# Kernel tuning notes

Measured on AMD Instinct MI355X. Metric: run time of the kernel, lower is better.

The kernel has to match this reference:

```python
import jax, jax.numpy as jnp
import numpy as np

N = 50000
E = 800000
IN_DIM = 512
H1 = IN_DIM // 2   # 256
H2 = IN_DIM // 4   # 128
D = 8
NP_CAYLEY = D * (D - 1) // 2  # 28


def setup_inputs() -> dict:
    key = jax.random.key(0)
    ks = jax.random.split(key, 10)
    x = jax.random.normal(ks[0], (N, IN_DIM), dtype=jnp.float32)
    edge_index = jax.random.randint(ks[1], (2, E), 0, N, dtype=jnp.int64)
    s1 = 1.0 / np.sqrt(IN_DIM)
    s2 = 1.0 / np.sqrt(H1)
    s3 = 1.0 / np.sqrt(H2)
    W1l = jax.random.uniform(ks[2], (H1, IN_DIM), jnp.float32, -s1, s1)
    b1 = jax.random.uniform(ks[3], (H1,), jnp.float32, -s1, s1)
    W1r = jax.random.uniform(ks[4], (H1, IN_DIM), jnp.float32, -s1, s1)
    W2l = jax.random.uniform(ks[5], (H2, H1), jnp.float32, -s2, s2)
    b2 = jax.random.uniform(ks[6], (H2,), jnp.float32, -s2, s2)
    W2r = jax.random.uniform(ks[7], (H2, H1), jnp.float32, -s2, s2)
    Wp = jax.random.uniform(ks[8], (NP_CAYLEY, H2), jnp.float32, -s3, s3)
    bp = jax.random.uniform(ks[9], (NP_CAYLEY,), jnp.float32, -s3, s3)
    return {"x": x, "edge_index": edge_index,
            "W1l": W1l, "b1": b1, "W1r": W1r,
            "W2l": W2l, "b2": b2, "W2r": W2r,
            "Wp": Wp, "bp": bp}


def _sage_conv(x, src, dst, Wl, bl, Wr):
    # PyG SAGEConv (mean aggr): out = lin_l(mean_{j in N(i)} x_j) + lin_r(x_i)
    msg_sum = jax.ops.segment_sum(x[src], dst, num_segments=N)  # [N, F]
    deg = jax.ops.segment_sum(jnp.ones((src.shape[0],), x.dtype), dst,
                              num_segments=N)
    mean = msg_sum / jnp.maximum(deg, 1.0)[:, None]
    return mean @ Wl.T + bl + x @ Wr.T


def _cayley(params):
    # params: [N, d(d-1)/2] -> skew A, then O = (I - A)^{-1} (I + A)
    iu, ju = jnp.triu_indices(D, k=1)  # row-major i<j matches torch loop order
    n = params.shape[0]
    A = jnp.zeros((n, D, D), params.dtype)
    A = A.at[:, iu, ju].set(params)
    A = A.at[:, ju, iu].set(-params)
    I = jnp.eye(D, dtype=params.dtype)
    return jnp.linalg.solve(I[None] - A, I[None] + A)


def reference(x, edge_index, W1l, b1, W1r, W2l, b2, W2r, Wp, bp):
    src, dst = edge_index[0], edge_index[1]
    h = jax.nn.relu(_sage_conv(x, src, dst, W1l, b1, W1r))
    h = jax.nn.relu(_sage_conv(h, src, dst, W2l, b2, W2r))
    params = h @ Wp.T + bp  # [N, 28]
    return _cayley(params)  # [N, 8, 8]
```

## Files before the change

### kernel.cpp

```cpp
#include <hip/hip_runtime.h>
#include <hip/hip_bf16.h>


#define WS_ALIGN(x) (((x) + 255) & ~size_t(255))

typedef __attribute__((ext_vector_type(8))) short short8;
typedef __attribute__((ext_vector_type(4))) float floatx4;

static __device__ __forceinline__ ushort f2b(float f) {
    unsigned u = __builtin_bit_cast(unsigned, f);
    u = (u + 0x7fffu + ((u >> 16) & 1u)) >> 16;
    return (ushort)u;
}
static __device__ __forceinline__ float b2f(ushort h) {
    unsigned u = ((unsigned)h) << 16;
    return __builtin_bit_cast(float, u);
}
static __device__ __forceinline__ unsigned pk2(float a, float b) {
    return (unsigned)f2b(a) | ((unsigned)f2b(b) << 16);
}


__global__ void hist_kernel(const int* __restrict__ dst, int* __restrict__ deg, int E) {
    int e = blockIdx.x * blockDim.x + threadIdx.x;
    if (e < E) atomicAdd(&deg[dst[e]], 1);
}

__global__ __launch_bounds__(256)
void scan_phase1(const int* __restrict__ deg, int* __restrict__ bsum, int n) {
    __shared__ int red[256];
    const int t = threadIdx.x;
    const int i = blockIdx.x * 1024 + t * 4;
    int s = 0;
    if (i + 4 <= n) {
        int4 v = *reinterpret_cast<const int4*>(&deg[i]);
        s = v.x + v.y + v.z + v.w;
    } else {
        for (int k = i; k < n; ++k) s += deg[k];
    }
    red[t] = s;
    __syncthreads();
#pragma unroll
    for (int off = 128; off > 0; off >>= 1) {
        if (t < off) red[t] += red[t + off];
        __syncthreads();
    }
    if (t == 0) bsum[blockIdx.x] = red[0];
}

__global__ __launch_bounds__(256)
void scan_phase2(int* __restrict__ bsum, int* __restrict__ rowptr, int nb, int n) {
    __shared__ int sh[256];
    const int t = threadIdx.x;
    int orig = (t < nb) ? bsum[t] : 0;
    sh[t] = orig;
    __syncthreads();
#pragma unroll
    for (int off = 1; off < 256; off <<= 1) {
        int v = (t >= off) ? sh[t - off] : 0;
        __syncthreads();
        sh[t] += v;
        __syncthreads();
    }
    if (t < nb) bsum[t] = sh[t] - orig;
    if (t == 255) rowptr[n] = sh[255];
}

__global__ __launch_bounds__(256)
void scan_phase3(const int* __restrict__ deg, const int* __restrict__ bsum,
                 int* __restrict__ rowptr, int n) {
    __shared__ int red[256];
    const int t = threadIdx.x;
    const int i = blockIdx.x * 1024 + t * 4;
    int v0 = 0, v1 = 0, v2 = 0, v3 = 0;
    if (i + 4 <= n) {
        int4 v = *reinterpret_cast<const int4*>(&deg[i]);
        v0 = v.x; v1 = v.y; v2 = v.z; v3 = v.w;
    } else {
        if (i     < n) v0 = deg[i];
        if (i + 1 < n) v1 = deg[i + 1];
        if (i + 2 < n) v2 = deg[i + 2];
        if (i + 3 < n) v3 = deg[i + 3];
    }
    int s = v0 + v1 + v2 + v3;
    red[t] = s;
    __syncthreads();
#pragma unroll
    for (int off = 1; off < 256; off <<= 1) {
        int u = (t >= off) ? red[t - off] : 0;
        __syncthreads();
        red[t] += u;
        __syncthreads();
    }
    int pre = bsum[blockIdx.x] + red[t] - s;
    if (i + 4 <= n) {
        int4 o;
        o.x = pre; o.y = pre + v0; o.z = pre + v0 + v1; o.w = pre + v0 + v1 + v2;
        *reinterpret_cast<int4*>(&rowptr[i]) = o;
    } else {
        if (i     < n) rowptr[i]     = pre;
        if (i + 1 < n) rowptr[i + 1] = pre + v0;
        if (i + 2 < n) rowptr[i + 2] = pre + v0 + v1;
        if (i + 3 < n) rowptr[i + 3] = pre + v0 + v1 + v2;
    }
}

__global__ void scatter_kernel(const int* __restrict__ src, const int* __restrict__ dst,
                               const int* __restrict__ rowptr, int* __restrict__ cursor,
                               int* __restrict__ adj, int E) {
    int e = blockIdx.x * blockDim.x + threadIdx.x;
    if (e < E) {
        int d = dst[e];
        int p = atomicAdd(&cursor[d], 1);
        adj[rowptr[d] + p] = src[e];
    }
}

__global__ void build_wcat(const float* __restrict__ W1l, const float* __restrict__ W1r,
                           const float* __restrict__ W2l, const float* __restrict__ W2r,
                           ushort* __restrict__ Wc1, ushort* __restrict__ Wc2) {
    int idx = blockIdx.x * blockDim.x + threadIdx.x;
    const int n1 = (512 * 512) / 8;
    const int n2 = (256 * 256) / 8;
    const float* src;
    ushort* dst;
    if (idx < n1) {
        int e = idx * 8;
        int row = e >> 9, col = e & 511;
        src = (row < 256) ? &W1l[row * 512 + col] : &W1r[(row - 256) * 512 + col];
        dst = &Wc1[e];
    } else if (idx < n1 + n2) {
        int e = (idx - n1) * 8;
        int row = e >> 8, col = e & 255;
        src = (row < 128) ? &W2l[row * 256 + col] : &W2r[(row - 128) * 256 + col];
        dst = &Wc2[e];
    } else {
        return;
    }
    const float4* s4 = reinterpret_cast<const float4*>(src);
    float4 v0 = s4[0], v1 = s4[1];
    short8 o;
    o[0] = (short)f2b(v0.x); o[1] = (short)f2b(v0.y);
    o[2] = (short)f2b(v0.z); o[3] = (short)f2b(v0.w);
    o[4] = (short)f2b(v1.x); o[5] = (short)f2b(v1.y);
    o[6] = (short)f2b(v1.z); o[7] = (short)f2b(v1.w);
    *reinterpret_cast<short8*>(dst) = o;
}


template <bool CASTA>
__global__ __launch_bounds__(256)
void gemm_db(const float* __restrict__ Af, const ushort* __restrict__ Ab,
             const ushort* __restrict__ B,
             ushort* __restrict__ Cl, ushort* __restrict__ Cr,
             int M, int K, int Ncols, int S) {
    __shared__ ushort As[2][128 * 64];
    __shared__ ushort Bs[2][128 * 64];
    const int tid  = threadIdx.x;
    const int wave = tid >> 6;
    const int lane = tid & 63;
    const int row0 = blockIdx.y * 128;
    const int col0 = blockIdx.x * 128;
    const int wm = (wave & 1) * 64;
    const int wn = (wave >> 1) * 64;

    floatx4 acc[4][4];
#pragma unroll
    for (int i = 0; i < 4; ++i)
#pragma unroll
        for (int j = 0; j < 4; ++j)
            acc[i][j] = (floatx4){0.f, 0.f, 0.f, 0.f};

    const int rsub = lane >> 3;
    const int ksw  = ((lane & 7) * 16) ^ (rsub << 4);

    const int ar = tid >> 1, ah = tid & 1;
    int agrow = row0 + ar; if (agrow >= M) agrow = M - 1;
    const float* arow = CASTA ? (Af + (size_t)agrow * K + ah * 32) : nullptr;
    const int arx = (ar & 7) << 4;
    float4 va[8];

    if constexpr (CASTA) {
#pragma unroll
        for (int j = 0; j < 8; ++j)
            va[j] = *reinterpret_cast<const float4*>(arow + j * 4);
    }
#pragma unroll
    for (int i = 0; i < 4; ++i) {
        int chunk = wave * 4 + i;
        int r = chunk * 8 + rsub;
        int gcol = col0 + r;
        const char* srcp = (const char*)(B + (size_t)gcol * K) + ksw;
        __builtin_amdgcn_global_load_lds(
            (const __attribute__((address_space(1))) unsigned int*)srcp,
            (__attribute__((address_space(3))) unsigned int*)(&Bs[0][chunk * 512]),
            16, 0, 0);
    }
    if constexpr (CASTA) {
        char* alds = (char*)&As[0][0] + ar * 128;
#pragma unroll
        for (int g = 0; g < 4; ++g) {
            uint4 o = make_uint4(pk2(va[2 * g].x, va[2 * g].y),
                                 pk2(va[2 * g].z, va[2 * g].w),
                                 pk2(va[2 * g + 1].x, va[2 * g + 1].y),
                                 pk2(va[2 * g + 1].z, va[2 * g + 1].w));
            *reinterpret_cast<uint4*>(alds + (((ah * 4 + g) * 16) ^ arx)) = o;
        }
    } else {
#pragma unroll
        for (int i = 0; i < 4; ++i) {
            int chunk = wave * 4 + i;
            int r = chunk * 8 + rsub;
            int grow = row0 + r;
            if (grow >= M) grow = M - 1;
            const char* srcp = (const char*)(Ab + (size_t)grow * K) + ksw;
            __builtin_amdgcn_global_load_lds(
                (const __attribute__((address_space(1))) unsigned int*)srcp,
                (__attribute__((address_space(3))) unsigned int*)(&As[0][chunk * 512]),
                16, 0, 0);
        }
    }
    __syncthreads();

    const int nt = K >> 6;
    int cur = 0;
#pragma unroll 2
    for (int t = 0; t < nt; ++t) {
        const int k0 = t * 64;
        const int nxt = cur ^ 1;
        const bool more = (t + 1 < nt);

        if (more) {
#pragma unroll
            for (int i = 0; i < 4; ++i) {
                int chunk = wave * 4 + i;
                int r = chunk * 8 + rsub;
                int gcol = col0 + r;
                const char* srcp = (const char*)(B + (size_t)gcol * K + k0 + 64) + ksw;
                __builtin_amdgcn_global_load_lds(
                    (const __attribute__((address_space(1))) unsigned int*)srcp,
                    (__attribute__((address_space(3))) unsigned int*)(&Bs[nxt][chunk * 512]),
                    16, 0, 0);
            }
            if constexpr (CASTA) {
                const float* s1 = arow + k0 + 64;
#pragma unroll
                for (int j = 0; j < 8; ++j)
                    va[j] = *reinterpret_cast<const float4*>(s1 + j * 4);
            } else {
#pragma unroll
                for (int i = 0; i < 4; ++i) {
                    int chunk = wave * 4 + i;
                    int r = chunk * 8 + rsub;
                    int grow = row0 + r;
                    if (grow >= M) grow = M - 1;
                    const char* srcp = (const char*)(Ab + (size_t)grow * K + k0 + 64) + ksw;
                    __builtin_amdgcn_global_load_lds(
                        (const __attribute__((address_space(1))) unsigned int*)srcp,
                        (__attribute__((address_space(3))) unsigned int*)(&As[nxt][chunk * 512]),
                        16, 0, 0);
                }
            }
        }

        const char* Al = (const char*)&As[cur][0];
        const char* Bl = (const char*)&Bs[cur][0];
#pragma unroll
        for (int kk = 0; kk < 2; ++kk) {
            short8 af[4], bf[4];
            const int kb = (kk * 64 + ((lane >> 4) << 4)) ^ ((lane & 7) << 4);
#pragma unroll
            for (int im = 0; im < 4; ++im) {
                int r = wm + im * 16 + (lane & 15);
                af[im] = *reinterpret_cast<const short8*>(Al + r * 128 + kb);
            }
#pragma unroll
            for (int in = 0; in < 4; ++in) {
                int r = wn + in * 16 + (lane & 15);
                bf[in] = *reinterpret_cast<const short8*>(Bl + r * 128 + kb);
            }
#pragma unroll
            for (int im = 0; im < 4; ++im)
#pragma unroll
                for (int in = 0; in < 4; ++in)
                    acc[im][in] = __builtin_amdgcn_mfma_f32_16x16x32_bf16(
                        af[im], bf[in], acc[im][in], 0, 0, 0);
        }

        if (CASTA && more) {
            char* alds = (char*)&As[cur ^ 1][0] + ar * 128;
#pragma unroll
            for (int g = 0; g < 4; ++g) {
                uint4 o = make_uint4(pk2(va[2 * g].x, va[2 * g].y),
                                     pk2(va[2 * g].z, va[2 * g].w),
                                     pk2(va[2 * g + 1].x, va[2 * g + 1].y),
                                     pk2(va[2 * g + 1].z, va[2 * g + 1].w));
                *reinterpret_cast<uint4*>(alds + (((ah * 4 + g) * 16) ^ arx)) = o;
            }
        }
        __syncthreads();
        cur ^= 1;
    }

    ushort* Cbase = (col0 < S) ? Cl : Cr;
    const int cb = (col0 < S) ? col0 : col0 - S;
#pragma unroll
    for (int im = 0; im < 4; ++im) {
#pragma unroll
        for (int reg = 0; reg < 4; ++reg) {
            int r = row0 + wm + im * 16 + ((lane >> 4) << 2) + reg;
            if (r < M) {
                size_t base = (size_t)r * S + cb + wn + (lane & 15);
#pragma unroll
                for (int in = 0; in < 4; ++in)
                    Cbase[base + in * 16] = f2b(acc[im][in][reg]);
            }
        }
    }
}


template <int LPN>
__global__ __launch_bounds__(256)
void aggregate_bf16(const ushort* __restrict__ Yl, const ushort* __restrict__ Yr,
                    const float* __restrict__ bias,
                    const int* __restrict__ rowptr, const int* __restrict__ adj,
                    ushort* __restrict__ H, int n) {
    constexpr int F = LPN * 8;
    const int grp = threadIdx.x / LPN;
    const int sub = threadIdx.x % LPN;
    const int node = blockIdx.x * (256 / LPN) + grp;
    if (node >= n) return;
    const int c = sub * 8;
    const int start = rowptr[node], end = rowptr[node + 1];

    float acc[8];
#pragma unroll
    for (int v = 0; v < 8; ++v) acc[v] = 0.f;

    int e = start;
    for (; e + 4 <= end; e += 4) {
        int s0 = adj[e + 0], s1 = adj[e + 1], s2 = adj[e + 2], s3 = adj[e + 3];
        short8 r0 = *reinterpret_cast<const short8*>(&Yl[(size_t)s0 * F + c]);
        short8 r1 = *reinterpret_cast<const short8*>(&Yl[(size_t)s1 * F + c]);
        short8 r2 = *reinterpret_cast<const short8*>(&Yl[(size_t)s2 * F + c]);
        short8 r3 = *reinterpret_cast<const short8*>(&Yl[(size_t)s3 * F + c]);
#pragma unroll
        for (int v = 0; v < 8; ++v)
            acc[v] += (b2f((ushort)r0[v]) + b2f((ushort)r1[v])) +
                      (b2f((ushort)r2[v]) + b2f((ushort)r3[v]));
    }
    for (; e < end; ++e) {
        int s = adj[e];
        short8 r = *reinterpret_cast<const short8*>(&Yl[(size_t)s * F + c]);
#pragma unroll
        for (int v = 0; v < 8; ++v) acc[v] += b2f((ushort)r[v]);
    }

    const int d = end - start;
    const float inv = 1.0f / (float)(d > 0 ? d : 1);
    short8 sv = *reinterpret_cast<const short8*>(&Yr[(size_t)node * F + c]);
    float4 bv0 = *reinterpret_cast<const float4*>(&bias[c]);
    float4 bv1 = *reinterpret_cast<const float4*>(&bias[c + 4]);
    float bb[8] = {bv0.x, bv0.y, bv0.z, bv0.w, bv1.x, bv1.y, bv1.z, bv1.w};
    short8 o;
#pragma unroll
    for (int v = 0; v < 8; ++v)
        o[v] = (short)f2b(fmaxf(acc[v] * inv + b2f((ushort)sv[v]) + bb[v], 0.f));
    *reinterpret_cast<short8*>(&H[(size_t)node * F + c]) = o;
}


__global__ __launch_bounds__(256)
void params_kernel(const ushort* __restrict__ H2, const float* __restrict__ Wp,
                   const float* __restrict__ bp, float* __restrict__ P, int n) {
    __shared__ float WpS[32 * 132];
    __shared__ float bpS[32];
    for (int t = threadIdx.x; t < 32 * 132; t += 256) WpS[t] = 0.f;
    if (threadIdx.x < 32) bpS[threadIdx.x] = (threadIdx.x < 28) ? bp[threadIdx.x] : 0.f;
    __syncthreads();
    for (int t = threadIdx.x; t < 28 * 128; t += 256) {
        int r = t >> 7, c = t & 127;
        WpS[r * 132 + c] = Wp[t];
    }
    __syncthreads();

    const int node = blockIdx.x * 32 + (threadIdx.x >> 3);
    const int l = threadIdx.x & 7;
    if (node >= n) return;

    short8 h8[16];
    const short8* hp = reinterpret_cast<const short8*>(&H2[(size_t)node * 128]);
#pragma unroll
    for (int q = 0; q < 16; ++q) h8[q] = hp[q];

    float acc0 = bpS[l], acc1 = bpS[l + 8], acc2 = bpS[l + 16], acc3 = bpS[l + 24];
#pragma unroll
    for (int q = 0; q < 32; ++q) {
        float h0 = b2f((ushort)h8[q >> 1][(q & 1) * 4 + 0]);
        float h1 = b2f((ushort)h8[q >> 1][(q & 1) * 4 + 1]);
        float h2 = b2f((ushort)h8[q >> 1][(q & 1) * 4 + 2]);
        float h3 = b2f((ushort)h8[q >> 1][(q & 1) * 4 + 3]);
        float4 w0 = *reinterpret_cast<const float4*>(&WpS[(l +  0) * 132 + 4 * q]);
        float4 w1 = *reinterpret_cast<const float4*>(&WpS[(l +  8) * 132 + 4 * q]);
        float4 w2 = *reinterpret_cast<const float4*>(&WpS[(l + 16) * 132 + 4 * q]);
        float4 w3 = *reinterpret_cast<const float4*>(&WpS[(l + 24) * 132 + 4 * q]);
        acc0 += h0 * w0.x + h1 * w0.y + h2 * w0.z + h3 * w0.w;
        acc1 += h0 * w1.x + h1 * w1.y + h2 * w1.z + h3 * w1.w;
        acc2 += h0 * w2.x + h1 * w2.y + h2 * w2.z + h3 * w2.w;
        acc3 += h0 * w3.x + h1 * w3.y + h2 * w3.z + h3 * w3.w;
    }
    float* pout = &P[(size_t)node * 32];
    pout[l]      = acc0;
    pout[l + 8]  = acc1;
    pout[l + 16] = acc2;
    pout[l + 24] = acc3;
}


__global__ __launch_bounds__(256)
void cayley_kernel(const float* __restrict__ P, float* __restrict__ Out, int n) {
    int i = blockIdx.x * blockDim.x + threadIdx.x;
    if (i >= n) return;
    float p[28];
    const float4* pp = reinterpret_cast<const float4*>(&P[(size_t)i * 32]);
#pragma unroll
    for (int q = 0; q < 7; ++q) {
        float4 v = pp[q];
        p[4 * q + 0] = v.x; p[4 * q + 1] = v.y;
        p[4 * q + 2] = v.z; p[4 * q + 3] = v.w;
    }

    float M_[8][8], B_[8][8];
#pragma unroll
    for (int r = 0; r < 8; ++r)
#pragma unroll
        for (int c = 0; c < 8; ++c) {
            M_[r][c] = (r == c) ? 1.f : 0.f;
            B_[r][c] = (r == c) ? 1.f : 0.f;
        }
    {
        int idx = 0;
#pragma unroll
        for (int r = 0; r < 8; ++r)
#pragma unroll
            for (int c = r + 1; c < 8; ++c) {
                float a = p[idx++];
                M_[r][c] -= a;  M_[c][r] += a;
                B_[r][c] += a;  B_[c][r] -= a;
            }
    }
#pragma unroll
    for (int col = 0; col < 8; ++col) {
        float inv = 1.0f / M_[col][col];
#pragma unroll
        for (int c = 0; c < 8; ++c) { M_[col][c] *= inv; B_[col][c] *= inv; }
#pragma unroll
        for (int r = 0; r < 8; ++r) {
            if (r == col) continue;
            float f = M_[r][col];
#pragma unroll
            for (int c = 0; c < 8; ++c) {
                M_[r][c] -= f * M_[col][c];
                B_[r][c] -= f * B_[col][c];
            }
        }
    }
    float* out = &Out[(size_t)i * 64];
#pragma unroll
    for (int r = 0; r < 8; ++r) {
        float4 o0 = make_float4(B_[r][0], B_[r][1], B_[r][2], B_[r][3]);
        float4 o1 = make_float4(B_[r][4], B_[r][5], B_[r][6], B_[r][7]);
        *reinterpret_cast<float4*>(&out[r * 8 + 0]) = o0;
        *reinterpret_cast<float4*>(&out[r * 8 + 4]) = o1;
    }
}


extern "C" void kernel_launch(void* const* d_in, const int* in_sizes, int n_in,
                              void* d_out, int out_size, void* d_ws, size_t ws_size,
                              hipStream_t stream) {
    const float* x   = (const float*)d_in[0];
    const int*   ei  = (const int*)d_in[1];
    const float* W1l = (const float*)d_in[2];
    const float* b1  = (const float*)d_in[3];
    const float* W1r = (const float*)d_in[4];
    const float* W2l = (const float*)d_in[5];
    const float* b2  = (const float*)d_in[6];
    const float* W2r = (const float*)d_in[7];
    const float* Wp  = (const float*)d_in[8];
    const float* bp  = (const float*)d_in[9];
    float* out = (float*)d_out;

    const int IN_DIM = 512;
    const int N = in_sizes[0] / IN_DIM;
    const int E = in_sizes[1] / 2;

    char* ws = (char*)d_ws;
    size_t off = 0;
    int* deg      = (int*)(ws + off); off = WS_ALIGN(off + (size_t)N * 4);
    int* rowptr   = (int*)(ws + off); off = WS_ALIGN(off + (size_t)(N + 1) * 4);
    int* cursor   = (int*)(ws + off); off = WS_ALIGN(off + (size_t)N * 4);
    int* bsum     = (int*)(ws + off); off = WS_ALIGN(off + (size_t)256 * 4);
    int* adj      = (int*)(ws + off); off = WS_ALIGN(off + (size_t)E * 4);
    ushort* Yl    = (ushort*)(ws + off); off = WS_ALIGN(off + (size_t)N * 256 * 2);
    ushort* Yr    = (ushort*)(ws + off); off = WS_ALIGN(off + (size_t)N * 256 * 2);
    ushort* h1    = (ushort*)(ws + off); off = WS_ALIGN(off + (size_t)N * 256 * 2);
    ushort* zl    = (ushort*)(ws + off); off = WS_ALIGN(off + (size_t)N * 128 * 2);
    ushort* zr    = (ushort*)(ws + off); off = WS_ALIGN(off + (size_t)N * 128 * 2);
    ushort* Wc1   = (ushort*)(ws + off); off = WS_ALIGN(off + (size_t)512 * 512 * 2);
    ushort* Wc2   = (ushort*)(ws + off); off = WS_ALIGN(off + (size_t)256 * 256 * 2);
    float*  Pp    = (float*)(ws + off);  off = WS_ALIGN(off + (size_t)N * 32 * 4);

    const int* src = ei;
    const int* dst = ei + E;

    hipMemsetAsync(deg, 0, (size_t)N * 4, stream);
    hipMemsetAsync(cursor, 0, (size_t)N * 4, stream);

    int eb = (E + 255) / 256;
    int nb = (N + 1023) / 1024;
    hist_kernel<<<eb, 256, 0, stream>>>(dst, deg, E);
    scan_phase1<<<nb, 256, 0, stream>>>(deg, bsum, N);
    scan_phase2<<<1, 256, 0, stream>>>(bsum, rowptr, nb, N);
    scan_phase3<<<nb, 256, 0, stream>>>(deg, bsum, rowptr, N);
    scatter_kernel<<<eb, 256, 0, stream>>>(src, dst, rowptr, cursor, adj, E);

    build_wcat<<<((512 * 512 + 256 * 256) / 8 + 255) / 256, 256, 0, stream>>>(
        W1l, W1r, W2l, W2r, Wc1, Wc2);

    int gm = (N + 127) / 128;

    gemm_db<true><<<dim3(4, gm), 256, 0, stream>>>(
        x, (const ushort*)nullptr, Wc1, Yl, Yr, N, 512, 512, 256);
    aggregate_bf16<32><<<(N + 7) / 8, 256, 0, stream>>>(Yl, Yr, b1, rowptr, adj, h1, N);

    gemm_db<false><<<dim3(2, gm), 256, 0, stream>>>(
        (const float*)nullptr, h1, Wc2, zl, zr, N, 256, 256, 128);
    ushort* h2 = Yl;
    aggregate_bf16<16><<<(N + 15) / 16, 256, 0, stream>>>(zl, zr, b2, rowptr, adj, h2, N);

    params_kernel<<<(N + 31) / 32, 256, 0, stream>>>(h2, Wp, bp, Pp, N);
    cayley_kernel<<<(N + 255) / 256, 256, 0, stream>>>(Pp, out, N);
}
```

Before: 317.4 us.

## Restructure GEMM pipeline with XCD-aware tile mapping and deeper aggregation unroll

Rewrites the two SAGE GEMMs as a compile-time-K kernel. It uses a 1D grid remapped so consecutive tiles land on the same XCD, a single LDS A buffer in the cast path (fp32 loads prefetched two tiles ahead), and launch bounds that target 3 blocks per CU. Together these aim to improve L2 locality, occupancy and load/compute overlap. The neighbor aggregation gains an 8-wide unrolled gather so more independent loads are in flight. The risks are extra barriers per k-step and higher register pressure from the larger unroll.

```diff
diff --git a/kernel.cpp b/kernel.cpp
--- a/kernel.cpp
+++ b/kernel.cpp
@@ -148,19 +148,28 @@
 }
 
 
-template <bool CASTA>
-__global__ __launch_bounds__(256)
-void gemm_db(const float* __restrict__ Af, const ushort* __restrict__ Ab,
+template <int KT, bool CASTA>
+__global__ __launch_bounds__(256, 3)
+void gemm_p2(const float* __restrict__ Af, const ushort* __restrict__ Ab,
              const ushort* __restrict__ B,
              ushort* __restrict__ Cl, ushort* __restrict__ Cr,
-             int M, int K, int Ncols, int S) {
-    __shared__ ushort As[2][128 * 64];
+             int M, int S, int gx) {
+    constexpr int nt = KT / 64;
+    constexpr int NA = CASTA ? 1 : 2;
+    __shared__ ushort As[NA][128 * 64];
     __shared__ ushort Bs[2][128 * 64];
+
     const int tid  = threadIdx.x;
     const int wave = tid >> 6;
     const int lane = tid & 63;
-    const int row0 = blockIdx.y * 128;
-    const int col0 = blockIdx.x * 128;
+
+    const int W = gridDim.x;
+    const int q = W >> 3, r = W & 7;
+    const int xcd = blockIdx.x & 7, slot = blockIdx.x >> 3;
+    const int w = (xcd < r ? xcd * (q + 1) : r * (q + 1) + (xcd - r) * q) + slot;
+    const int row0 = (w / gx) * 128;
+    const int col0 = (w % gx) * 128;
+
     const int wm = (wave & 1) * 64;
     const int wn = (wave >> 1) * 64;
 
@@ -176,27 +185,43 @@
 
     const int ar = tid >> 1, ah = tid & 1;
     int agrow = row0 + ar; if (agrow >= M) agrow = M - 1;
-    const float* arow = CASTA ? (Af + (size_t)agrow * K + ah * 32) : nullptr;
+    const float* arow = CASTA ? (Af + (size_t)agrow * KT + ah * 32) : nullptr;
     const int arx = (ar & 7) << 4;
     float4 va[8];
 
-    if constexpr (CASTA) {
+    auto stageB = [&](int t, int buf) {
+#pragma unroll
+        for (int i = 0; i < 4; ++i) {
+            int chunk = wave * 4 + i;
+            int rr = chunk * 8 + rsub;
+            const char* srcp = (const char*)(B + (size_t)(col0 + rr) * KT + t * 64) + ksw;
+            __builtin_amdgcn_global_load_lds(
+                (const __attribute__((address_space(1))) unsigned int*)srcp,
+                (__attribute__((address_space(3))) unsigned int*)(&Bs[buf][chunk * 512]),
+                16, 0, 0);
+        }
+    };
+    auto stageA_dma = [&](int t, int buf) {
+#pragma unroll
+        for (int i = 0; i < 4; ++i) {
+            int chunk = wave * 4 + i;
+            int rr = chunk * 8 + rsub;
+            int grow = row0 + rr;
+            if (grow >= M) grow = M - 1;
+            const char* srcp = (const char*)(Ab + (size_t)grow * KT + t * 64) + ksw;
+            __builtin_amdgcn_global_load_lds(
+                (const __attribute__((address_space(1))) unsigned int*)srcp,
+                (__attribute__((address_space(3))) unsigned int*)(&As[buf][chunk * 512]),
+                16, 0, 0);
+        }
+    };
+    auto loadA = [&](int t) {
+        const float* s = arow + t * 64;
 #pragma unroll
         for (int j = 0; j < 8; ++j)
-            va[j] = *reinterpret_cast<const float4*>(arow + j * 4);
-    }
-#pragma unroll
-    for (int i = 0; i < 4; ++i) {
-        int chunk = wave * 4 + i;
-        int r = chunk * 8 + rsub;
-        int gcol = col0 + r;
-        const char* srcp = (const char*)(B + (size_t)gcol * K) + ksw;
-        __builtin_amdgcn_global_load_lds(
-            (const __attribute__((address_space(1))) unsigned int*)srcp,
-            (__attribute__((address_space(3))) unsigned int*)(&Bs[0][chunk * 512]),
-            16, 0, 0);
-    }
-    if constexpr (CASTA) {
+            va[j] = *reinterpret_cast<const float4*>(s + j * 4);
+    };
+    auto packA = [&]() {
         char* alds = (char*)&As[0][0] + ar * 128;
 #pragma unroll
         for (int g = 0; g < 4; ++g) {
@@ -206,64 +231,26 @@
                                  pk2(va[2 * g + 1].z, va[2 * g + 1].w));
             *reinterpret_cast<uint4*>(alds + (((ah * 4 + g) * 16) ^ arx)) = o;
         }
+    };
+
+    if constexpr (CASTA) loadA(0);
+    stageB(0, 0);
+    if constexpr (CASTA) {
+        packA();
+        if (nt > 1) loadA(1);
     } else {
-#pragma unroll
-        for (int i = 0; i < 4; ++i) {
-            int chunk = wave * 4 + i;
-            int r = chunk * 8 + rsub;
-            int grow = row0 + r;
-            if (grow >= M) grow = M - 1;
-            const char* srcp = (const char*)(Ab + (size_t)grow * K) + ksw;
-            __builtin_amdgcn_global_load_lds(
-                (const __attribute__((address_space(1))) unsigned int*)srcp,
-                (__attribute__((address_space(3))) unsigned int*)(&As[0][chunk * 512]),
-                16, 0, 0);
-        }
+        stageA_dma(0, 0);
     }
     __syncthreads();
 
-    const int nt = K >> 6;
-    int cur = 0;
-#pragma unroll 2
+#pragma unroll
     for (int t = 0; t < nt; ++t) {
-        const int k0 = t * 64;
-        const int nxt = cur ^ 1;
-        const bool more = (t + 1 < nt);
-
-        if (more) {
-#pragma unroll
-            for (int i = 0; i < 4; ++i) {
-                int chunk = wave * 4 + i;
-                int r = chunk * 8 + rsub;
-                int gcol = col0 + r;
-                const char* srcp = (const char*)(B + (size_t)gcol * K + k0 + 64) + ksw;
-                __builtin_amdgcn_global_load_lds(
-                    (const __attribute__((address_space(1))) unsigned int*)srcp,
-                    (__attribute__((address_space(3))) unsigned int*)(&Bs[nxt][chunk * 512]),
-                    16, 0, 0);
-            }
-            if constexpr (CASTA) {
-                const float* s1 = arow + k0 + 64;
-#pragma unroll
-                for (int j = 0; j < 8; ++j)
-                    va[j] = *reinterpret_cast<const float4*>(s1 + j * 4);
-            } else {
-#pragma unroll
-                for (int i = 0; i < 4; ++i) {
-                    int chunk = wave * 4 + i;
-                    int r = chunk * 8 + rsub;
-                    int grow = row0 + r;
-                    if (grow >= M) grow = M - 1;
-                    const char* srcp = (const char*)(Ab + (size_t)grow * K + k0 + 64) + ksw;
-                    __builtin_amdgcn_global_load_lds(
-                        (const __attribute__((address_space(1))) unsigned int*)srcp,
-                        (__attribute__((address_space(3))) unsigned int*)(&As[nxt][chunk * 512]),
-                        16, 0, 0);
-                }
-            }
-        }
-
-        const char* Al = (const char*)&As[cur][0];
+        const int cur = t & 1, nxt = cur ^ 1;
+        if (t + 1 < nt) {
+            stageB(t + 1, nxt);
+            if constexpr (!CASTA) stageA_dma(t + 1, nxt);
+        }
+        const char* Al = (const char*)&As[CASTA ? 0 : cur][0];
         const char* Bl = (const char*)&Bs[cur][0];
 #pragma unroll
         for (int kk = 0; kk < 2; ++kk) {
@@ -271,13 +258,13 @@
             const int kb = (kk * 64 + ((lane >> 4) << 4)) ^ ((lane & 7) << 4);
 #pragma unroll
             for (int im = 0; im < 4; ++im) {
-                int r = wm + im * 16 + (lane & 15);
-                af[im] = *reinterpret_cast<const short8*>(Al + r * 128 + kb);
+                int rr = wm + im * 16 + (lane & 15);
+                af[im] = *reinterpret_cast<const short8*>(Al + rr * 128 + kb);
             }
 #pragma unroll
             for (int in = 0; in < 4; ++in) {
-                int r = wn + in * 16 + (lane & 15);
-                bf[in] = *reinterpret_cast<const short8*>(Bl + r * 128 + kb);
+                int rr = wn + in * 16 + (lane & 15);
+                bf[in] = *reinterpret_cast<const short8*>(Bl + rr * 128 + kb);
             }
 #pragma unroll
             for (int im = 0; im < 4; ++im)
@@ -286,20 +273,17 @@
                     acc[im][in] = __builtin_amdgcn_mfma_f32_16x16x32_bf16(
                         af[im], bf[in], acc[im][in], 0, 0, 0);
         }
-
-        if (CASTA && more) {
-            char* alds = (char*)&As[cur ^ 1][0] + ar * 128;
-#pragma unroll
-            for (int g = 0; g < 4; ++g) {
-                uint4 o = make_uint4(pk2(va[2 * g].x, va[2 * g].y),
-                                     pk2(va[2 * g].z, va[2 * g].w),
-                                     pk2(va[2 * g + 1].x, va[2 * g + 1].y),
-                                     pk2(va[2 * g + 1].z, va[2 * g + 1].w));
-                *reinterpret_cast<uint4*>(alds + (((ah * 4 + g) * 16) ^ arx)) = o;
+        __syncthreads();
+        if constexpr (CASTA) {
+            if (t + 1 < nt) {
+                packA();
+                if (t + 2 < nt) loadA(t + 2);
+                __builtin_amdgcn_sched_barrier(0);
+                asm volatile("s_waitcnt lgkmcnt(0)" ::: "memory");
+                __builtin_amdgcn_s_barrier();
+                __builtin_amdgcn_sched_barrier(0);
             }
         }
-        __syncthreads();
-        cur ^= 1;
     }
 
     ushort* Cbase = (col0 < S) ? Cl : Cr;
@@ -308,9 +292,9 @@
     for (int im = 0; im < 4; ++im) {
 #pragma unroll
         for (int reg = 0; reg < 4; ++reg) {
-            int r = row0 + wm + im * 16 + ((lane >> 4) << 2) + reg;
-            if (r < M) {
-                size_t base = (size_t)r * S + cb + wn + (lane & 15);
+            int rr = row0 + wm + im * 16 + ((lane >> 4) << 2) + reg;
+            if (rr < M) {
+                size_t base = (size_t)rr * S + cb + wn + (lane & 15);
 #pragma unroll
                 for (int in = 0; in < 4; ++in)
                     Cbase[base + in * 16] = f2b(acc[im][in][reg]);
@@ -339,6 +323,22 @@
     for (int v = 0; v < 8; ++v) acc[v] = 0.f;
 
     int e = start;
+    for (; e + 8 <= end; e += 8) {
+        short8 rr[8];
+#pragma unroll
+        for (int u = 0; u < 8; ++u) {
+            int s = adj[e + u];
+            rr[u] = *reinterpret_cast<const short8*>(&Yl[(size_t)s * F + c]);
+        }
+#pragma unroll
+        for (int v = 0; v < 8; ++v) {
+            float t0 = (b2f((ushort)rr[0][v]) + b2f((ushort)rr[1][v])) +
+                       (b2f((ushort)rr[2][v]) + b2f((ushort)rr[3][v]));
+            float t1 = (b2f((ushort)rr[4][v]) + b2f((ushort)rr[5][v])) +
+                       (b2f((ushort)rr[6][v]) + b2f((ushort)rr[7][v]));
+            acc[v] += t0 + t1;
+        }
+    }
     for (; e + 4 <= end; e += 4) {
         int s0 = adj[e + 0], s1 = adj[e + 1], s2 = adj[e + 2], s3 = adj[e + 3];
         short8 r0 = *reinterpret_cast<const short8*>(&Yl[(size_t)s0 * F + c]);
@@ -352,9 +352,9 @@
     }
     for (; e < end; ++e) {
         int s = adj[e];
-        short8 r = *reinterpret_cast<const short8*>(&Yl[(size_t)s * F + c]);
-#pragma unroll
-        for (int v = 0; v < 8; ++v) acc[v] += b2f((ushort)r[v]);
+        short8 rr = *reinterpret_cast<const short8*>(&Yl[(size_t)s * F + c]);
+#pragma unroll
+        for (int v = 0; v < 8; ++v) acc[v] += b2f((ushort)rr[v]);
     }
 
     const int d = end - start;
@@ -531,12 +531,12 @@
 
     int gm = (N + 127) / 128;
 
-    gemm_db<true><<<dim3(4, gm), 256, 0, stream>>>(
-        x, (const ushort*)nullptr, Wc1, Yl, Yr, N, 512, 512, 256);
+    gemm_p2<512, true><<<gm * 4, 256, 0, stream>>>(
+        x, (const ushort*)nullptr, Wc1, Yl, Yr, N, 256, 4);
     aggregate_bf16<32><<<(N + 7) / 8, 256, 0, stream>>>(Yl, Yr, b1, rowptr, adj, h1, N);
 
-    gemm_db<false><<<dim3(2, gm), 256, 0, stream>>>(
-        (const float*)nullptr, h1, Wc2, zl, zr, N, 256, 256, 128);
+    gemm_p2<256, false><<<gm * 2, 256, 0, stream>>>(
+        (const float*)nullptr, h1, Wc2, zl, zr, N, 128, 2);
     ushort* h2 = Yl;
     aggregate_bf16<16><<<(N + 15) / 16, 256, 0, stream>>>(zl, zr, b2, rowptr, adj, h2, N);
 
```

Measured after the change: 307.4 us. 3.1% less time.
